# Performance work log

Measured on AMD Instinct MI355X. Metric: run time of the kernel, lower is better.

Reference implementation:

```python
import jax, jax.numpy as jnp
import numpy as np

DIM = 1024
HEADS = 16
DIM_HEAD = 64
INNER = HEADS * DIM_HEAD  # 1024
FF_INNER = 4 * DIM        # 4096
EPS = 1e-5


def _ln(t, gamma):
    mu = jnp.mean(t, axis=-1, keepdims=True)
    var = jnp.var(t, axis=-1, keepdims=True)
    return (t - mu) * jax.lax.rsqrt(var + EPS) * gamma


def setup_inputs() -> dict:
    key = jax.random.key(0)
    ks = jax.random.split(key, 8)
    B, N = 4, 1024
    s = 0.02
    return {
        "x": jax.random.normal(ks[0], (B, N, DIM), dtype=jnp.float32),
        "y": jax.random.normal(ks[1], (B, N, DIM), dtype=jnp.float32),
        "g1": jnp.ones((DIM,), dtype=jnp.float32),
        "g2": jnp.ones((DIM,), dtype=jnp.float32),
        "g_out": jnp.ones((DIM,), dtype=jnp.float32),
        "Wq": jax.random.normal(ks[2], (DIM, INNER), dtype=jnp.float32) * s,
        "Wkv": jax.random.normal(ks[3], (DIM, 2 * DIM_HEAD), dtype=jnp.float32) * s,
        "Wo": jax.random.normal(ks[4], (INNER, DIM), dtype=jnp.float32) * s,
        "Wff1": jax.random.normal(ks[5], (DIM, 2 * FF_INNER), dtype=jnp.float32) * s,
        "Wff2": jax.random.normal(ks[6], (FF_INNER, DIM), dtype=jnp.float32) * s,
    }


def reference(x, y, g1, g2, g_out, Wq, Wkv, Wo, Wff1, Wff2):
    B, N, _ = x.shape
    scale = DIM_HEAD ** -0.5
    xn = _ln(x, g1)
    yn = _ln(y, g2)  # note: torch code rebinds y = norm2(y); residual & FF use normed y
    # multi-query attention: per-head queries, single shared k/v head
    q = (xn @ Wq).reshape(B, N, HEADS, DIM_HEAD).transpose(0, 2, 1, 3) * scale  # b h n d
    kv = yn @ Wkv  # b j (2d)
    k, v = kv[..., :DIM_HEAD], kv[..., DIM_HEAD:]
    sim = jnp.einsum('bhid,bjd->bhij', q, k)
    attn = jax.nn.softmax(sim, axis=-1)  # torch code subtracts amax then softmax; identical math
    out = jnp.einsum('bhij,bjd->bhid', attn, v)
    out = out.transpose(0, 2, 1, 3).reshape(B, N, INNER)
    out = out @ Wo
    out = _ln(out + yn, g_out)
    # SwiGLU FFN on normed y: first half is value, second half is gate
    h = yn @ Wff1
    val, gate = h[..., :FF_INNER], h[..., FF_INNER:]
    ff = (jax.nn.silu(gate) * val) @ Wff2
    return out + ff
```

## Files before the change

kernel.cpp:

```cpp
#include <hip/hip_runtime.h>
#include <hip/hip_bf16.h>


typedef __attribute__((ext_vector_type(8))) short bf16x8;
typedef __attribute__((ext_vector_type(4))) short s16x4;
typedef __attribute__((ext_vector_type(4))) float f32x4;

__device__ __forceinline__ short f2b(float f) {
  union { float f; unsigned u; } v; v.f = f;
  unsigned r = (v.u + 0x7fffu + ((v.u >> 16) & 1u)) >> 16;
  return (short)r;
}

__device__ __forceinline__ void gload16(const short* g, short* l) {
  __builtin_amdgcn_global_load_lds(
      (const __attribute__((address_space(1))) void*)g,
      (__attribute__((address_space(3))) void*)l, 16, 0, 0);
}

__global__ __launch_bounds__(256) void cvtT_kernel(const float* __restrict__ in,
                                                   short* __restrict__ out,
                                                   int K, int N) {
  __shared__ float tile[32][33];
  int n0 = blockIdx.x * 32, k0 = blockIdx.y * 32;
  int tx = threadIdx.x & 7, ty = threadIdx.x >> 3;
  float4 v = *(const float4*)&in[(size_t)(k0 + ty) * N + n0 + tx * 4];
  tile[ty][tx * 4 + 0] = v.x;
  tile[ty][tx * 4 + 1] = v.y;
  tile[ty][tx * 4 + 2] = v.z;
  tile[ty][tx * 4 + 3] = v.w;
  __syncthreads();
  s16x4 o = { f2b(tile[tx * 4 + 0][ty]), f2b(tile[tx * 4 + 1][ty]),
              f2b(tile[tx * 4 + 2][ty]), f2b(tile[tx * 4 + 3][ty]) };
  *(s16x4*)&out[(size_t)(n0 + ty) * K + k0 + tx * 4] = o;
}

__global__ __launch_bounds__(256) void ln_kernel(const float* __restrict__ in,
                                                 const float* __restrict__ gamma,
                                                 short* __restrict__ out16,
                                                 float* __restrict__ out32) {
  int row = blockIdx.x;
  int t = threadIdx.x;
  float4 v = ((const float4*)(in + (size_t)row * 1024))[t];
  float s  = v.x + v.y + v.z + v.w;
  float sq = v.x*v.x + v.y*v.y + v.z*v.z + v.w*v.w;
  __shared__ float ssum[256], ssq[256];
  ssum[t] = s; ssq[t] = sq;
  __syncthreads();
  for (int o = 128; o > 0; o >>= 1) {
    if (t < o) { ssum[t] += ssum[t + o]; ssq[t] += ssq[t + o]; }
    __syncthreads();
  }
  float mu  = ssum[0] * (1.0f / 1024.0f);
  float var = ssq[0] * (1.0f / 1024.0f) - mu * mu;
  float rs  = rsqrtf(var + 1e-5f);
  float4 g = ((const float4*)gamma)[t];
  float o0 = (v.x - mu) * rs * g.x;
  float o1 = (v.y - mu) * rs * g.y;
  float o2 = (v.z - mu) * rs * g.z;
  float o3 = (v.w - mu) * rs * g.w;
  if (out16) {
    s16x4 o = { f2b(o0), f2b(o1), f2b(o2), f2b(o3) };
    ((s16x4*)out16)[(size_t)row * 256 + t] = o;
  }
  if (out32) {
    float4 o = { o0, o1, o2, o3 };
    ((float4*)out32)[(size_t)row * 256 + t] = o;
  }
}

template<int EPI, bool DUAL>
__global__ __launch_bounds__(256, 2) void gemm_ring(
    const short* __restrict__ A, const short* __restrict__ B,
    int M, int N, int K,
    short* __restrict__ out16, float* __restrict__ out32,
    const float* __restrict__ res, float scale)
{
  constexpr int DEPTH = DUAL ? 3 : 4;
  __shared__ __align__(16) short As[DEPTH][128 * 32];
  __shared__ __align__(16) short Bs[DEPTH][128 * 32];
  __shared__ __align__(16) short Bs2[DUAL ? DEPTH : 1][DUAL ? 128 * 32 : 8];

  int t = threadIdx.x;
  int lane = t & 63, wave = t >> 6;
  int wm = wave >> 1, wn = wave & 1;
  int lrow = lane & 15, lgrp = lane >> 4;
  int m0 = blockIdx.y * 128, n0 = blockIdx.x * 128;

  int srow = lane >> 2, scol = (lane & 3) * 8;
  const short* gA  = A + (size_t)(m0 + wave * 16 + srow) * K + scol;
  const short* gB  = B + (size_t)(n0 + wave * 16 + srow) * K + scol;
  const short* gB2 = DUAL ? B + (size_t)(4096 + n0 + wave * 16 + srow) * K + scol : gB;

  auto STAGE = [&](int slot, int kt) {
    int k0 = kt * 32;
    gload16(gA + k0,                  &As[slot][wave * 512]);
    gload16(gA + (size_t)64 * K + k0, &As[slot][(wave + 4) * 512]);
    gload16(gB + k0,                  &Bs[slot][wave * 512]);
    gload16(gB + (size_t)64 * K + k0, &Bs[slot][(wave + 4) * 512]);
    if constexpr (DUAL) {
      gload16(gB2 + k0,                  &Bs2[slot][wave * 512]);
      gload16(gB2 + (size_t)64 * K + k0, &Bs2[slot][(wave + 4) * 512]);
    }
  };

  f32x4 acc[4][4];
  f32x4 acc2[4][4];
  const f32x4 zero = { 0.f, 0.f, 0.f, 0.f };
#pragma unroll
  for (int i = 0; i < 4; i++)
#pragma unroll
    for (int j = 0; j < 4; j++) { acc[i][j] = zero; if (DUAL) acc2[i][j] = zero; }

  int nt = K / 32;
#pragma unroll
  for (int p = 0; p < DEPTH - 1; p++) STAGE(p, p);

  int slot = 0, stage_slot = (DEPTH - 1) % DEPTH;
  for (int tI = 0; tI < nt; ++tI) {
    int rem = nt - 1 - tI;
    if constexpr (DUAL) {
      if (rem >= 1) asm volatile("s_waitcnt vmcnt(6)" ::: "memory");
      else          asm volatile("s_waitcnt vmcnt(0)" ::: "memory");
    } else {
      if (rem >= 2)      asm volatile("s_waitcnt vmcnt(8)" ::: "memory");
      else if (rem == 1) asm volatile("s_waitcnt vmcnt(4)" ::: "memory");
      else               asm volatile("s_waitcnt vmcnt(0)" ::: "memory");
    }
    __builtin_amdgcn_s_barrier();

    if (tI + DEPTH - 1 < nt) STAGE(stage_slot, tI + DEPTH - 1);

    bf16x8 af[4], bfr[4], bfr2[4];
#pragma unroll
    for (int mf = 0; mf < 4; mf++)
      af[mf] = *(const bf16x8*)&As[slot][(wm * 64 + mf * 16 + lrow) * 32 + lgrp * 8];
#pragma unroll
    for (int nf = 0; nf < 4; nf++)
      bfr[nf] = *(const bf16x8*)&Bs[slot][(wn * 64 + nf * 16 + lrow) * 32 + lgrp * 8];
    if constexpr (DUAL) {
#pragma unroll
      for (int nf = 0; nf < 4; nf++)
        bfr2[nf] = *(const bf16x8*)&Bs2[slot][(wn * 64 + nf * 16 + lrow) * 32 + lgrp * 8];
    }
    asm volatile("s_waitcnt lgkmcnt(0)" ::: "memory");
    __builtin_amdgcn_sched_barrier(0);

    __builtin_amdgcn_s_setprio(1);
#pragma unroll
    for (int mf = 0; mf < 4; mf++)
#pragma unroll
      for (int nf = 0; nf < 4; nf++) {
        acc[mf][nf] = __builtin_amdgcn_mfma_f32_16x16x32_bf16(af[mf], bfr[nf], acc[mf][nf], 0, 0, 0);
        if constexpr (DUAL)
          acc2[mf][nf] = __builtin_amdgcn_mfma_f32_16x16x32_bf16(af[mf], bfr2[nf], acc2[mf][nf], 0, 0, 0);
      }
    __builtin_amdgcn_s_setprio(0);

    slot = (slot + 1 == DEPTH) ? 0 : slot + 1;
    stage_slot = (stage_slot + 1 == DEPTH) ? 0 : stage_slot + 1;
  }

#pragma unroll
  for (int mf = 0; mf < 4; mf++)
#pragma unroll
    for (int nf = 0; nf < 4; nf++)
#pragma unroll
      for (int r = 0; r < 4; r++) {
        int row = m0 + wm * 64 + mf * 16 + lgrp * 4 + r;
        int col = n0 + wn * 64 + nf * 16 + lrow;
        float v = acc[mf][nf][r];
        if (EPI == 0) {
          out16[(size_t)row * N + col] = f2b(v * scale);
        } else if (EPI == 1) {
          out32[(size_t)row * N + col] = v + res[(size_t)row * N + col];
        } else {
          float gate = acc2[mf][nf][r];
          float sig = 1.0f / (1.0f + __expf(-gate));
          out16[(size_t)row * N + col] = f2b(v * gate * sig);
        }
      }
}

__global__ __launch_bounds__(256) void attn_kernel(const short* __restrict__ q,
                                                   const short* __restrict__ kv,
                                                   short* __restrict__ ao)
{
  __shared__ __align__(16) short Ks[64 * 64];
  __shared__ __align__(16) short Vs[64 * 64];
  __shared__ __align__(16) short Ps[4][32 * 64];

  int t = threadIdx.x;
  int lane = t & 63, wave = t >> 6;
  int lrow = lane & 15, lgrp = lane >> 4;
  int qt = blockIdx.x;
  int b = blockIdx.y >> 2, hg = blockIdx.y & 3;
  int h = hg * 4 + wave;

  char* Kb = (char*)Ks;
  char* Vb = (char*)Vs;
  char* Pb = (char*)Ps + wave * (32 * 64 * 2);

  bf16x8 qf[2][2];
  const short* qb = q + ((size_t)(b * 1024 + qt * 32)) * 1024 + h * 64;
#pragma unroll
  for (int mf = 0; mf < 2; mf++)
#pragma unroll
    for (int kk = 0; kk < 2; kk++)
      qf[mf][kk] = *(const bf16x8*)&qb[(size_t)(mf * 16 + lrow) * 1024 + kk * 32 + lgrp * 8];

  f32x4 oacc[2][4];
  float m_[2][4], l_[2][4];
  const f32x4 zero = { 0.f, 0.f, 0.f, 0.f };
#pragma unroll
  for (int i = 0; i < 2; i++)
#pragma unroll
    for (int j = 0; j < 4; j++) { oacc[i][j] = zero; }
#pragma unroll
  for (int i = 0; i < 2; i++)
#pragma unroll
    for (int r = 0; r < 4; r++) { m_[i][r] = -3.0e38f; l_[i][r] = 0.f; }

  int4 d[4];
  {
    const short* kvb = kv + ((size_t)(b * 1024 + lane)) * 128 + wave * 32;
#pragma unroll
    for (int i = 0; i < 4; i++) d[i] = ((const int4*)kvb)[i];
  }

  for (int j0 = 0; j0 < 1024; j0 += 64) {
    __syncthreads();
    if (wave < 2) {
      int sw = (lane & 7) << 4;
#pragma unroll
      for (int i = 0; i < 4; i++)
        *(int4*)(Kb + lane * 128 + ((wave * 64 + i * 16) ^ sw)) = d[i];
    } else {
#pragma unroll
      for (int i = 0; i < 4; i++) {
        union { int4 v; short s[8]; } u; u.v = d[i];
#pragma unroll
        for (int j = 0; j < 8; j++) {
          int dd = (wave - 2) * 32 + i * 8 + j;
          *(short*)(Vb + dd * 128 + ((lane * 2) ^ ((dd & 7) << 4))) = u.s[j];
        }
      }
    }
    if (j0 + 64 < 1024) {
      const short* kvn = kv + ((size_t)(b * 1024 + j0 + 64 + lane)) * 128 + wave * 32;
#pragma unroll
      for (int i = 0; i < 4; i++) d[i] = ((const int4*)kvn)[i];
    }
    __syncthreads();

    bf16x8 kf[4][2];
#pragma unroll
    for (int nf = 0; nf < 4; nf++) {
      int row = nf * 16 + lrow, sw = (row & 7) << 4;
      kf[nf][0] = *(const bf16x8*)(Kb + row * 128 + ((lgrp * 16) ^ sw));
      kf[nf][1] = *(const bf16x8*)(Kb + row * 128 + ((64 + lgrp * 16) ^ sw));
    }
    f32x4 sacc[2][4];
#pragma unroll
    for (int i = 0; i < 2; i++)
#pragma unroll
      for (int j = 0; j < 4; j++) sacc[i][j] = zero;
    __builtin_amdgcn_s_setprio(1);
#pragma unroll
    for (int mf = 0; mf < 2; mf++)
#pragma unroll
      for (int nf = 0; nf < 4; nf++)
#pragma unroll
        for (int kk = 0; kk < 2; kk++)
          sacc[mf][nf] = __builtin_amdgcn_mfma_f32_16x16x32_bf16(qf[mf][kk], kf[nf][kk], sacc[mf][nf], 0, 0, 0);
    __builtin_amdgcn_s_setprio(0);

    float pmax[2][4];
    bool okd = true;
#pragma unroll
    for (int mf = 0; mf < 2; mf++)
#pragma unroll
      for (int r = 0; r < 4; r++) {
        float pm = fmaxf(fmaxf(sacc[mf][0][r], sacc[mf][1][r]),
                         fmaxf(sacc[mf][2][r], sacc[mf][3][r]));
        pmax[mf][r] = pm;
        okd = okd && (pm <= m_[mf][r] + 8.0f);
      }
    if (__all(okd)) {
#pragma unroll
      for (int mf = 0; mf < 2; mf++)
#pragma unroll
        for (int r = 0; r < 4; r++) {
          int row = mf * 16 + lgrp * 4 + r, sw = (row & 7) << 4;
          float al = 0.f;
#pragma unroll
          for (int nf = 0; nf < 4; nf++) {
            float p = __expf(sacc[mf][nf][r] - m_[mf][r]);
            *(short*)(Pb + row * 128 + (((nf * 16 + lrow) * 2) ^ sw)) = f2b(p);
            al += p;
          }
          l_[mf][r] += al;
        }
    } else {
#pragma unroll
      for (int mf = 0; mf < 2; mf++)
#pragma unroll
        for (int r = 0; r < 4; r++) {
          float mx = pmax[mf][r];
#pragma unroll
          for (int o = 8; o >= 1; o >>= 1) mx = fmaxf(mx, __shfl_xor(mx, o));
          float mnew = fmaxf(m_[mf][r], mx);
          float corr = __expf(m_[mf][r] - mnew);
          int row = mf * 16 + lgrp * 4 + r, sw = (row & 7) << 4;
          float al = 0.f;
#pragma unroll
          for (int nf = 0; nf < 4; nf++) {
            float p = __expf(sacc[mf][nf][r] - mnew);
            *(short*)(Pb + row * 128 + (((nf * 16 + lrow) * 2) ^ sw)) = f2b(p);
            al += p;
          }
          l_[mf][r] = l_[mf][r] * corr + al;
          m_[mf][r] = mnew;
#pragma unroll
          for (int nf = 0; nf < 4; nf++) oacc[mf][nf][r] *= corr;
        }
    }

    bf16x8 vf[4][2], pf[2][2];
#pragma unroll
    for (int nf = 0; nf < 4; nf++) {
      int row = nf * 16 + lrow, sw = (row & 7) << 4;
      vf[nf][0] = *(const bf16x8*)(Vb + row * 128 + ((lgrp * 16) ^ sw));
      vf[nf][1] = *(const bf16x8*)(Vb + row * 128 + ((64 + lgrp * 16) ^ sw));
    }
#pragma unroll
    for (int mf = 0; mf < 2; mf++) {
      int row = mf * 16 + lrow, sw = (row & 7) << 4;
      pf[mf][0] = *(const bf16x8*)(Pb + row * 128 + ((lgrp * 16) ^ sw));
      pf[mf][1] = *(const bf16x8*)(Pb + row * 128 + ((64 + lgrp * 16) ^ sw));
    }
    __builtin_amdgcn_s_setprio(1);
#pragma unroll
    for (int mf = 0; mf < 2; mf++)
#pragma unroll
      for (int nf = 0; nf < 4; nf++)
#pragma unroll
        for (int kk = 0; kk < 2; kk++)
          oacc[mf][nf] = __builtin_amdgcn_mfma_f32_16x16x32_bf16(pf[mf][kk], vf[nf][kk], oacc[mf][nf], 0, 0, 0);
    __builtin_amdgcn_s_setprio(0);
  }

#pragma unroll
  for (int mf = 0; mf < 2; mf++)
#pragma unroll
    for (int r = 0; r < 4; r++) {
      float ls = l_[mf][r];
#pragma unroll
      for (int o = 8; o >= 1; o >>= 1) ls += __shfl_xor(ls, o);
      float inv = 1.0f / ls;
      int qrow = qt * 32 + mf * 16 + lgrp * 4 + r;
#pragma unroll
      for (int nf = 0; nf < 4; nf++) {
        float val = oacc[mf][nf][r] * inv;
        ao[((size_t)(b * 1024 + qrow)) * 1024 + h * 64 + nf * 16 + lrow] = f2b(val);
      }
    }
}

extern "C" void kernel_launch(void* const* d_in, const int* in_sizes, int n_in,
                              void* d_out, int out_size, void* d_ws, size_t ws_size,
                              hipStream_t stream) {
  const float* x     = (const float*)d_in[0];
  const float* y     = (const float*)d_in[1];
  const float* g1    = (const float*)d_in[2];
  const float* g2    = (const float*)d_in[3];
  const float* g_out = (const float*)d_in[4];
  const float* Wq    = (const float*)d_in[5];
  const float* Wkv   = (const float*)d_in[6];
  const float* Wo    = (const float*)d_in[7];
  const float* Wff1  = (const float*)d_in[8];
  const float* Wff2  = (const float*)d_in[9];

  char* ws = (char*)d_ws;
  size_t off = 0;
  auto alloc = [&](size_t bytes) { char* p = ws + off; off += bytes; return p; };
  short* wqT    = (short*)alloc((size_t)1024 * 1024 * 2);
  short* wkvT   = (short*)alloc((size_t)128 * 1024 * 2);
  short* woT    = (short*)alloc((size_t)1024 * 1024 * 2);
  short* wff1T  = (short*)alloc((size_t)8192 * 1024 * 2);
  short* wff2T  = (short*)alloc((size_t)1024 * 4096 * 2);
  short* xn16   = (short*)alloc((size_t)4096 * 1024 * 2);
  short* yn16   = (short*)alloc((size_t)4096 * 1024 * 2);
  float* ynf    = (float*)alloc((size_t)4096 * 1024 * 4);
  short* q16    = (short*)alloc((size_t)4096 * 1024 * 2);
  short* kv16   = (short*)alloc((size_t)4096 * 128 * 2);
  short* ao16   = (short*)alloc((size_t)4096 * 1024 * 2);
  float* lnout  = (float*)alloc((size_t)4096 * 1024 * 4);
  short* act16  = (short*)alloc((size_t)4096 * 4096 * 2);
  float* outf   = (float*)d_out;

  cvtT_kernel<<<dim3(1024 / 32, 1024 / 32), 256, 0, stream>>>(Wq,   wqT,   1024, 1024);
  cvtT_kernel<<<dim3(128 / 32, 1024 / 32),  256, 0, stream>>>(Wkv,  wkvT,  1024, 128);
  cvtT_kernel<<<dim3(1024 / 32, 1024 / 32), 256, 0, stream>>>(Wo,   woT,   1024, 1024);
  cvtT_kernel<<<dim3(8192 / 32, 1024 / 32), 256, 0, stream>>>(Wff1, wff1T, 1024, 8192);
  cvtT_kernel<<<dim3(1024 / 32, 4096 / 32), 256, 0, stream>>>(Wff2, wff2T, 4096, 1024);

  ln_kernel<<<4096, 256, 0, stream>>>(x, g1, xn16, nullptr);
  ln_kernel<<<4096, 256, 0, stream>>>(y, g2, yn16, ynf);

  gemm_ring<0, false><<<dim3(8, 32), 256, 0, stream>>>(
      xn16, wqT, 4096, 1024, 1024, q16, nullptr, nullptr, 0.125f);
  gemm_ring<0, false><<<dim3(1, 32), 256, 0, stream>>>(
      yn16, wkvT, 4096, 128, 1024, kv16, nullptr, nullptr, 1.0f);

  attn_kernel<<<dim3(32, 16), 256, 0, stream>>>(q16, kv16, ao16);

  gemm_ring<1, false><<<dim3(8, 32), 256, 0, stream>>>(
      ao16, woT, 4096, 1024, 1024, nullptr, outf, ynf, 1.0f);

  ln_kernel<<<4096, 256, 0, stream>>>(outf, g_out, nullptr, lnout);

  gemm_ring<2, true><<<dim3(32, 32), 256, 0, stream>>>(
      yn16, wff1T, 4096, 4096, 1024, act16, nullptr, nullptr, 1.0f);

  gemm_ring<1, false><<<dim3(8, 32), 256, 0, stream>>>(
      act16, wff2T, 4096, 1024, 4096, nullptr, outf, lnout, 1.0f);
}
```

Baseline: 351.7 us.

## Template GEMM tile size, use 64x128 tiles, split-K the KV projection

Makes the GEMM tile shape a template parameter and switches the Q, output-projection and FF2 GEMMs to 64x128 tiles, doubling the block count to fill more compute units. The small KV projection (which launched only 32 blocks) is split four ways along K into fp32 partials, followed by a new reduction kernel that sums them and converts to bf16. The explicit lgkmcnt wait after the LDS fragment loads is removed and a sched_barrier is added after the s_barrier. The trade-off is less reuse per tile, an extra launch and extra partial-sum traffic.

```diff
diff --git a/kernel.cpp b/kernel.cpp
--- a/kernel.cpp
+++ b/kernel.cpp
@@ -69,88 +69,100 @@
   }
 }
 
-template<int EPI, bool DUAL>
+template<int EPI, bool DUAL, int BM, int BN>
 __global__ __launch_bounds__(256, 2) void gemm_ring(
     const short* __restrict__ A, const short* __restrict__ B,
-    int M, int N, int K,
+    int M, int N, int Kstride, int Klen,
     short* __restrict__ out16, float* __restrict__ out32,
     const float* __restrict__ res, float scale)
 {
   constexpr int DEPTH = DUAL ? 3 : 4;
-  __shared__ __align__(16) short As[DEPTH][128 * 32];
-  __shared__ __align__(16) short Bs[DEPTH][128 * 32];
-  __shared__ __align__(16) short Bs2[DUAL ? DEPTH : 1][DUAL ? 128 * 32 : 8];
+  constexpr int FM = BM / 32;
+  constexpr int FN = BN / 32;
+  constexpr int AL = BM / 64;
+  constexpr int BL = BN / 64;
+  constexpr int LPT = AL + BL * (DUAL ? 2 : 1);
+  __shared__ __align__(16) short As[DEPTH][BM * 32];
+  __shared__ __align__(16) short Bs[DEPTH][BN * 32];
+  __shared__ __align__(16) short Bs2[DUAL ? DEPTH : 1][DUAL ? BN * 32 : 8];
 
   int t = threadIdx.x;
   int lane = t & 63, wave = t >> 6;
   int wm = wave >> 1, wn = wave & 1;
   int lrow = lane & 15, lgrp = lane >> 4;
-  int m0 = blockIdx.y * 128, n0 = blockIdx.x * 128;
+  int m0 = blockIdx.y * BM, n0 = blockIdx.x * BN;
+  int kbase = blockIdx.z * Klen;
 
   int srow = lane >> 2, scol = (lane & 3) * 8;
-  const short* gA  = A + (size_t)(m0 + wave * 16 + srow) * K + scol;
-  const short* gB  = B + (size_t)(n0 + wave * 16 + srow) * K + scol;
-  const short* gB2 = DUAL ? B + (size_t)(4096 + n0 + wave * 16 + srow) * K + scol : gB;
+  const short* gA  = A + (size_t)(m0 + wave * 16 + srow) * Kstride + kbase + scol;
+  const short* gB  = B + (size_t)(n0 + wave * 16 + srow) * Kstride + kbase + scol;
+  const short* gB2 = DUAL ? B + (size_t)(4096 + n0 + wave * 16 + srow) * Kstride + kbase + scol : gB;
 
   auto STAGE = [&](int slot, int kt) {
     int k0 = kt * 32;
-    gload16(gA + k0,                  &As[slot][wave * 512]);
-    gload16(gA + (size_t)64 * K + k0, &As[slot][(wave + 4) * 512]);
-    gload16(gB + k0,                  &Bs[slot][wave * 512]);
-    gload16(gB + (size_t)64 * K + k0, &Bs[slot][(wave + 4) * 512]);
+#pragma unroll
+    for (int i = 0; i < AL; i++)
+      gload16(gA + (size_t)(i * 64) * Kstride + k0, &As[slot][(i * 4 + wave) * 512]);
+#pragma unroll
+    for (int j = 0; j < BL; j++)
+      gload16(gB + (size_t)(j * 64) * Kstride + k0, &Bs[slot][(j * 4 + wave) * 512]);
     if constexpr (DUAL) {
-      gload16(gB2 + k0,                  &Bs2[slot][wave * 512]);
-      gload16(gB2 + (size_t)64 * K + k0, &Bs2[slot][(wave + 4) * 512]);
+#pragma unroll
+      for (int j = 0; j < BL; j++)
+        gload16(gB2 + (size_t)(j * 64) * Kstride + k0, &Bs2[slot][(j * 4 + wave) * 512]);
     }
   };
 
-  f32x4 acc[4][4];
-  f32x4 acc2[4][4];
+  f32x4 acc[FM][FN];
+  f32x4 acc2[DUAL ? FM : 1][DUAL ? FN : 1];
   const f32x4 zero = { 0.f, 0.f, 0.f, 0.f };
 #pragma unroll
-  for (int i = 0; i < 4; i++)
-#pragma unroll
-    for (int j = 0; j < 4; j++) { acc[i][j] = zero; if (DUAL) acc2[i][j] = zero; }
-
-  int nt = K / 32;
+  for (int i = 0; i < FM; i++)
+#pragma unroll
+    for (int j = 0; j < FN; j++) { acc[i][j] = zero; if (DUAL) acc2[i][j] = zero; }
+
+  int nt = Klen / 32;
 #pragma unroll
   for (int p = 0; p < DEPTH - 1; p++) STAGE(p, p);
 
-  int slot = 0, stage_slot = (DEPTH - 1) % DEPTH;
+  int slot = 0, stage_slot = DEPTH - 1;
   for (int tI = 0; tI < nt; ++tI) {
     int rem = nt - 1 - tI;
     if constexpr (DUAL) {
       if (rem >= 1) asm volatile("s_waitcnt vmcnt(6)" ::: "memory");
       else          asm volatile("s_waitcnt vmcnt(0)" ::: "memory");
-    } else {
+    } else if constexpr (LPT == 4) {
       if (rem >= 2)      asm volatile("s_waitcnt vmcnt(8)" ::: "memory");
       else if (rem == 1) asm volatile("s_waitcnt vmcnt(4)" ::: "memory");
       else               asm volatile("s_waitcnt vmcnt(0)" ::: "memory");
+    } else {
+      if (rem >= 2)      asm volatile("s_waitcnt vmcnt(6)" ::: "memory");
+      else if (rem == 1) asm volatile("s_waitcnt vmcnt(3)" ::: "memory");
+      else               asm volatile("s_waitcnt vmcnt(0)" ::: "memory");
     }
     __builtin_amdgcn_s_barrier();
+    __builtin_amdgcn_sched_barrier(0);
 
     if (tI + DEPTH - 1 < nt) STAGE(stage_slot, tI + DEPTH - 1);
 
-    bf16x8 af[4], bfr[4], bfr2[4];
-#pragma unroll
-    for (int mf = 0; mf < 4; mf++)
-      af[mf] = *(const bf16x8*)&As[slot][(wm * 64 + mf * 16 + lrow) * 32 + lgrp * 8];
-#pragma unroll
-    for (int nf = 0; nf < 4; nf++)
-      bfr[nf] = *(const bf16x8*)&Bs[slot][(wn * 64 + nf * 16 + lrow) * 32 + lgrp * 8];
+    bf16x8 af[FM], bfr[FN], bfr2[DUAL ? FN : 1];
+#pragma unroll
+    for (int mf = 0; mf < FM; mf++)
+      af[mf] = *(const bf16x8*)&As[slot][(wm * (BM / 2) + mf * 16 + lrow) * 32 + lgrp * 8];
+#pragma unroll
+    for (int nf = 0; nf < FN; nf++)
+      bfr[nf] = *(const bf16x8*)&Bs[slot][(wn * (BN / 2) + nf * 16 + lrow) * 32 + lgrp * 8];
     if constexpr (DUAL) {
 #pragma unroll
-      for (int nf = 0; nf < 4; nf++)
-        bfr2[nf] = *(const bf16x8*)&Bs2[slot][(wn * 64 + nf * 16 + lrow) * 32 + lgrp * 8];
-    }
-    asm volatile("s_waitcnt lgkmcnt(0)" ::: "memory");
-    __builtin_amdgcn_sched_barrier(0);
+      for (int nf = 0; nf < FN; nf++)
+        bfr2[nf] = *(const bf16x8*)&Bs2[slot][(wn * (BN / 2) + nf * 16 + lrow) * 32 + lgrp * 8];
+    }
 
     __builtin_amdgcn_s_setprio(1);
 #pragma unroll
-    for (int mf = 0; mf < 4; mf++)
-#pragma unroll
-      for (int nf = 0; nf < 4; nf++) {
+    for (int mf = 0; mf < FM; mf++)
+#pragma unroll
+      for (int nf = 0; nf < FN; nf++) {
         acc[mf][nf] = __builtin_amdgcn_mfma_f32_16x16x32_bf16(af[mf], bfr[nf], acc[mf][nf], 0, 0, 0);
         if constexpr (DUAL)
           acc2[mf][nf] = __builtin_amdgcn_mfma_f32_16x16x32_bf16(af[mf], bfr2[nf], acc2[mf][nf], 0, 0, 0);
@@ -162,24 +174,40 @@
   }
 
 #pragma unroll
-  for (int mf = 0; mf < 4; mf++)
-#pragma unroll
-    for (int nf = 0; nf < 4; nf++)
+  for (int mf = 0; mf < FM; mf++)
+#pragma unroll
+    for (int nf = 0; nf < FN; nf++)
 #pragma unroll
       for (int r = 0; r < 4; r++) {
-        int row = m0 + wm * 64 + mf * 16 + lgrp * 4 + r;
-        int col = n0 + wn * 64 + nf * 16 + lrow;
+        int row = m0 + wm * (BM / 2) + mf * 16 + lgrp * 4 + r;
+        int col = n0 + wn * (BN / 2) + nf * 16 + lrow;
         float v = acc[mf][nf][r];
         if (EPI == 0) {
           out16[(size_t)row * N + col] = f2b(v * scale);
         } else if (EPI == 1) {
           out32[(size_t)row * N + col] = v + res[(size_t)row * N + col];
+        } else if (EPI == 3) {
+          out32[(size_t)blockIdx.z * M * N + (size_t)row * N + col] = v;
         } else {
           float gate = acc2[mf][nf][r];
           float sig = 1.0f / (1.0f + __expf(-gate));
           out16[(size_t)row * N + col] = f2b(v * gate * sig);
         }
       }
+}
+
+__global__ __launch_bounds__(256) void kvred_kernel(const float* __restrict__ p,
+                                                    short* __restrict__ out, int n4) {
+  int i = blockIdx.x * 256 + threadIdx.x;
+  if (i >= n4) return;
+  const int S = 4096 * 128 / 4;
+  float4 a = ((const float4*)p)[i];
+  float4 b = ((const float4*)p)[i + S];
+  float4 c = ((const float4*)p)[i + 2 * S];
+  float4 d = ((const float4*)p)[i + 3 * S];
+  s16x4 o = { f2b(a.x + b.x + c.x + d.x), f2b(a.y + b.y + c.y + d.y),
+              f2b(a.z + b.z + c.z + d.z), f2b(a.w + b.w + c.w + d.w) };
+  ((s16x4*)out)[i] = o;
 }
 
 __global__ __launch_bounds__(256) void attn_kernel(const short* __restrict__ q,
@@ -397,6 +425,7 @@
   short* ao16   = (short*)alloc((size_t)4096 * 1024 * 2);
   float* lnout  = (float*)alloc((size_t)4096 * 1024 * 4);
   short* act16  = (short*)alloc((size_t)4096 * 4096 * 2);
+  float* kvpart = (float*)alloc((size_t)4 * 4096 * 128 * 4);
   float* outf   = (float*)d_out;
 
   cvtT_kernel<<<dim3(1024 / 32, 1024 / 32), 256, 0, stream>>>(Wq,   wqT,   1024, 1024);
@@ -408,21 +437,22 @@
   ln_kernel<<<4096, 256, 0, stream>>>(x, g1, xn16, nullptr);
   ln_kernel<<<4096, 256, 0, stream>>>(y, g2, yn16, ynf);
 
-  gemm_ring<0, false><<<dim3(8, 32), 256, 0, stream>>>(
-      xn16, wqT, 4096, 1024, 1024, q16, nullptr, nullptr, 0.125f);
-  gemm_ring<0, false><<<dim3(1, 32), 256, 0, stream>>>(
-      yn16, wkvT, 4096, 128, 1024, kv16, nullptr, nullptr, 1.0f);
+  gemm_ring<0, false, 64, 128><<<dim3(8, 64), 256, 0, stream>>>(
+      xn16, wqT, 4096, 1024, 1024, 1024, q16, nullptr, nullptr, 0.125f);
+  gemm_ring<3, false, 64, 128><<<dim3(1, 64, 4), 256, 0, stream>>>(
+      yn16, wkvT, 4096, 128, 1024, 256, nullptr, kvpart, nullptr, 1.0f);
+  kvred_kernel<<<512, 256, 0, stream>>>(kvpart, kv16, 4096 * 128 / 4);
 
   attn_kernel<<<dim3(32, 16), 256, 0, stream>>>(q16, kv16, ao16);
 
-  gemm_ring<1, false><<<dim3(8, 32), 256, 0, stream>>>(
-      ao16, woT, 4096, 1024, 1024, nullptr, outf, ynf, 1.0f);
+  gemm_ring<1, false, 64, 128><<<dim3(8, 64), 256, 0, stream>>>(
+      ao16, woT, 4096, 1024, 1024, 1024, nullptr, outf, ynf, 1.0f);
 
   ln_kernel<<<4096, 256, 0, stream>>>(outf, g_out, nullptr, lnout);
 
-  gemm_ring<2, true><<<dim3(32, 32), 256, 0, stream>>>(
-      yn16, wff1T, 4096, 4096, 1024, act16, nullptr, nullptr, 1.0f);
-
-  gemm_ring<1, false><<<dim3(8, 32), 256, 0, stream>>>(
-      act16, wff2T, 4096, 1024, 4096, nullptr, outf, lnout, 1.0f);
-}
+  gemm_ring<2, true, 128, 128><<<dim3(32, 32), 256, 0, stream>>>(
+      yn16, wff1T, 4096, 4096, 1024, 1024, act16, nullptr, nullptr, 1.0f);
+
+  gemm_ring<1, false, 64, 128><<<dim3(8, 64), 256, 0, stream>>>(
+      act16, wff2T, 4096, 1024, 4096, 4096, nullptr, outf, lnout, 1.0f);
+}
```

Result: faster. 325.4 us (-7.5%).
